# Kernel optimization log

Hardware: AMD Instinct MI355X
Metric: run time of the kernel (lower is better)

Reference implementation:

```python
import jax, jax.numpy as jnp
import numpy as np

N_NODES = 100000
N_EDGES = 1200000
D_FEAT = 64


def setup_inputs() -> dict:
    key = jax.random.key(0)
    k1, k2, k3 = jax.random.split(key, 3)
    x = jax.random.normal(k1, (N_NODES, D_FEAT), dtype=jnp.float32)
    edge_index = jax.random.randint(k2, (2, N_EDGES), 0, N_NODES, dtype=jnp.int64)
    edge_weight = jax.random.uniform(k3, (N_EDGES, 1), dtype=jnp.float32)
    return {"x": x, "edge_index": edge_index, "edge_weight": edge_weight}


def reference(x, edge_index, edge_weight):
    # flow = source_to_target: j = edge_index[0] (source), i = edge_index[1] (target)
    src, dst = edge_index[0], edge_index[1]
    # message: x_j  (gather along node_dim=-2)
    msg = x[src]                       # [E, D]
    # aggregate: scatter-'sum' with edge_weight scaling
    msg = msg * edge_weight            # [E, D]
    out = jax.ops.segment_sum(msg, dst, num_segments=N_NODES)  # [N, D]
    # update: identity
    return out
```

## Files before the change

### kernel.cpp

```cpp
#include <hip/hip_runtime.h>
#include <hip/hip_bf16.h>


constexpr int D_FEAT        = 64;
constexpr int BIN_SHIFT     = 7;
constexpr int NODES_PER_BIN = 1 << BIN_SHIFT;
constexpr int NBINS_MAX     = 1024;
constexpr int BIN_CAP       = 2048;
constexpr int EPB           = 4096;
constexpr int OVF_CAP       = 32768;

__device__ __forceinline__ int wave_incl_scan(int v, int lane) {
    #pragma unroll
    for (int d = 1; d < 64; d <<= 1) {
        int t = __shfl_up(v, d);
        if (lane >= d) v += t;
    }
    return v;
}

__device__ __forceinline__ unsigned short f32_to_bf16_rn(float f) {
    unsigned int u = __float_as_uint(f);
    u += 0x7FFFu + ((u >> 16) & 1u);
    return (unsigned short)(u >> 16);
}

__global__ __launch_bounds__(256) void mp_convert(
    const float* __restrict__ x, ushort* __restrict__ xb, int n4)
{
    const int i = blockIdx.x * blockDim.x + threadIdx.x;
    if (i < n4) {
        const float4 v = reinterpret_cast<const float4*>(x)[i];
        ushort4 o;
        o.x = f32_to_bf16_rn(v.x);
        o.y = f32_to_bf16_rn(v.y);
        o.z = f32_to_bf16_rn(v.z);
        o.w = f32_to_bf16_rn(v.w);
        reinterpret_cast<ushort4*>(xb)[i] = o;
    }
}

__global__ __launch_bounds__(1024) void mp_partition(
    const int* __restrict__ src, const int* __restrict__ dst,
    const float* __restrict__ w,
    int*  __restrict__ gcnt,
    int2* __restrict__ payload,
    int*  __restrict__ ovf_cnt, int4* __restrict__ ovf,
    int n_edges, int nbins)
{
    __shared__ int cnt[NBINS_MAX];
    __shared__ int start[NBINS_MAX];
    __shared__ int cur[NBINS_MAX];
    __shared__ int gbase[NBINS_MAX];
    __shared__ unsigned short binof[EPB];
    __shared__ int2 sorted[EPB];
    __shared__ int wsum[16];

    const int t    = threadIdx.x;
    const int lane = t & 63;
    const int wid  = t >> 6;
    const int base = blockIdx.x * EPB;
    const int nblk = min(EPB, n_edges - base);

    if (t < NBINS_MAX) cnt[t] = 0;
    __syncthreads();

    const int i4 = (base >> 2) + t;
    int4 d4 = make_int4(0, 0, 0, 0);
    bool have = (i4 * 4 < n_edges);
    if (have) {
        d4 = reinterpret_cast<const int4*>(dst)[i4];
        atomicAdd(&cnt[d4.x >> BIN_SHIFT], 1);
        atomicAdd(&cnt[d4.y >> BIN_SHIFT], 1);
        atomicAdd(&cnt[d4.z >> BIN_SHIFT], 1);
        atomicAdd(&cnt[d4.w >> BIN_SHIFT], 1);
    }
    __syncthreads();

    const int c = (t < nbins) ? cnt[t] : 0;
    const int incl = wave_incl_scan(c, lane);
    if (lane == 63) wsum[wid] = incl;
    __syncthreads();
    int woff = 0;
    #pragma unroll
    for (int k = 0; k < 16; ++k) woff += (k < wid) ? wsum[k] : 0;
    const int excl = woff + incl - c;
    if (t < nbins) {
        start[t] = excl;
        cur[t]   = excl;
        if (c > 0) gbase[t] = atomicAdd(&gcnt[t], c);
    }
    __syncthreads();

    if (have) {
        const int4   s4 = reinterpret_cast<const int4*>(src)[i4];
        const float4 w4 = reinterpret_cast<const float4*>(w)[i4];
        const int   dd[4] = {d4.x, d4.y, d4.z, d4.w};
        const int   ss[4] = {s4.x, s4.y, s4.z, s4.w};
        const float ww[4] = {w4.x, w4.y, w4.z, w4.w};
        #pragma unroll
        for (int j = 0; j < 4; ++j) {
            const int b   = dd[j] >> BIN_SHIFT;
            const int low = dd[j] & (NODES_PER_BIN - 1);
            const int p   = atomicAdd(&cur[b], 1);
            sorted[p] = make_int2((low << 20) | ss[j], __float_as_int(ww[j]));
            binof[p]  = (unsigned short)b;
        }
    }
    __syncthreads();

    #pragma unroll
    for (int k = 0; k < EPB / 1024; ++k) {
        const int i = k * 1024 + t;
        if (i >= nblk) break;
        const int b    = binof[i];
        const int idx  = i - start[b];
        const int gpos = gbase[b] + idx;
        const int2 e   = sorted[i];
        if (gpos < BIN_CAP) {
            payload[(size_t)b * BIN_CAP + gpos] = e;
        } else {
            const int op = atomicAdd(ovf_cnt, 1);
            if (op < OVF_CAP)
                ovf[op] = make_int4((b << BIN_SHIFT) + (e.x >> 20),
                                    e.x & 0xFFFFF, e.y, 0);
        }
    }
}

__global__ __launch_bounds__(512) void mp_bin_gather(
    const ushort* __restrict__ xb,
    const float*  __restrict__ x,
    const int*  __restrict__ gcnt,
    const int2* __restrict__ payload,
    const int*  __restrict__ ovf_cnt, const int4* __restrict__ ovf,
    float* __restrict__ out, int n_nodes)
{
    __shared__ int2 sraw[BIN_CAP];
    __shared__ int2 sedge[BIN_CAP];
    __shared__ int ncnt[NODES_PER_BIN];
    __shared__ int nstart[NODES_PER_BIN + 1];
    __shared__ int ncur[NODES_PER_BIN];

    const int b    = blockIdx.x;
    const int t    = threadIdx.x;
    const int lane = t & 63;
    const int wid  = t >> 6;
    const int sub  = lane >> 3;
    const int fg   = (lane & 7) * 8;

    const int m = min(gcnt[b], BIN_CAP);
    const int2* pl = payload + (size_t)b * BIN_CAP;

    for (int i = t; i < NODES_PER_BIN; i += 512) ncnt[i] = 0;
    __syncthreads();

    for (int i = t; i < m; i += 512) {
        const int2 e = pl[i];
        sraw[i] = e;
        atomicAdd(&ncnt[e.x >> 20], 1);
    }
    __syncthreads();

    if (t < 64) {
        const int a0 = ncnt[t], a1 = ncnt[64 + t];
        const int s0 = wave_incl_scan(a0, t);
        const int s1 = wave_incl_scan(a1, t);
        const int tot0 = __shfl(s0, 63);
        nstart[t]      = s0 - a0;
        nstart[64 + t] = tot0 + s1 - a1;
        if (t == 63) nstart[128] = tot0 + s1;
    }
    __syncthreads();
    for (int i = t; i < NODES_PER_BIN; i += 512) ncur[i] = nstart[i];
    __syncthreads();

    for (int i = t; i < m; i += 512) {
        const int2 e = sraw[i];
        const int p  = atomicAdd(&ncur[e.x >> 20], 1);
        sedge[p] = e;
    }
    __syncthreads();

    const int novf = *ovf_cnt;

    for (int n = wid; n < NODES_PER_BIN; n += 8) {
        const int node = (b << BIN_SHIFT) + n;
        if (node >= n_nodes) break;
        const int s0 = nstart[n], s1 = nstart[n + 1];

        float a0 = 0.f, a1 = 0.f, a2 = 0.f, a3 = 0.f;
        float a4 = 0.f, a5 = 0.f, a6 = 0.f, a7 = 0.f;

        int base = s0;
        for (; base + 8 <= s1; base += 8) {
            const int2 p = sedge[base + sub];
            const uint4 xv = *reinterpret_cast<const uint4*>(
                xb + (size_t)(p.x & 0xFFFFF) * D_FEAT + fg);
            const float ww = __int_as_float(p.y);
            a0 = fmaf(__uint_as_float(xv.x << 16),          ww, a0);
            a1 = fmaf(__uint_as_float(xv.x & 0xFFFF0000u),  ww, a1);
            a2 = fmaf(__uint_as_float(xv.y << 16),          ww, a2);
            a3 = fmaf(__uint_as_float(xv.y & 0xFFFF0000u),  ww, a3);
            a4 = fmaf(__uint_as_float(xv.z << 16),          ww, a4);
            a5 = fmaf(__uint_as_float(xv.z & 0xFFFF0000u),  ww, a5);
            a6 = fmaf(__uint_as_float(xv.w << 16),          ww, a6);
            a7 = fmaf(__uint_as_float(xv.w & 0xFFFF0000u),  ww, a7);
        }
        const int rem = s1 - base;
        if (sub < rem) {
            const int2 p = sedge[base + sub];
            const uint4 xv = *reinterpret_cast<const uint4*>(
                xb + (size_t)(p.x & 0xFFFFF) * D_FEAT + fg);
            const float ww = __int_as_float(p.y);
            a0 = fmaf(__uint_as_float(xv.x << 16),          ww, a0);
            a1 = fmaf(__uint_as_float(xv.x & 0xFFFF0000u),  ww, a1);
            a2 = fmaf(__uint_as_float(xv.y << 16),          ww, a2);
            a3 = fmaf(__uint_as_float(xv.y & 0xFFFF0000u),  ww, a3);
            a4 = fmaf(__uint_as_float(xv.z << 16),          ww, a4);
            a5 = fmaf(__uint_as_float(xv.z & 0xFFFF0000u),  ww, a5);
            a6 = fmaf(__uint_as_float(xv.w << 16),          ww, a6);
            a7 = fmaf(__uint_as_float(xv.w & 0xFFFF0000u),  ww, a7);
        }

        #pragma unroll
        for (int mask = 8; mask <= 32; mask <<= 1) {
            a0 += __shfl_xor(a0, mask); a1 += __shfl_xor(a1, mask);
            a2 += __shfl_xor(a2, mask); a3 += __shfl_xor(a3, mask);
            a4 += __shfl_xor(a4, mask); a5 += __shfl_xor(a5, mask);
            a6 += __shfl_xor(a6, mask); a7 += __shfl_xor(a7, mask);
        }

        if (sub == 0) {
            if (novf > 0) {
                const int lim = min(novf, OVF_CAP);
                for (int j = 0; j < lim; ++j) {
                    const int4 o = ovf[j];
                    if (o.x == node) {
                        const float* xr = x + (size_t)o.y * D_FEAT + fg;
                        const float ww = __int_as_float(o.z);
                        a0 = fmaf(xr[0], ww, a0); a1 = fmaf(xr[1], ww, a1);
                        a2 = fmaf(xr[2], ww, a2); a3 = fmaf(xr[3], ww, a3);
                        a4 = fmaf(xr[4], ww, a4); a5 = fmaf(xr[5], ww, a5);
                        a6 = fmaf(xr[6], ww, a6); a7 = fmaf(xr[7], ww, a7);
                    }
                }
            }
            float* orow = out + (size_t)node * D_FEAT + fg;
            *reinterpret_cast<float4*>(orow)     = make_float4(a0, a1, a2, a3);
            *reinterpret_cast<float4*>(orow + 4) = make_float4(a4, a5, a6, a7);
        }
    }
}

__global__ __launch_bounds__(256) void mp_scatter_atomic(
    const float* __restrict__ x, const int* __restrict__ src,
    const int* __restrict__ dst, const float* __restrict__ w,
    float* __restrict__ out, int n_edges)
{
    const int gtid = blockIdx.x * blockDim.x + threadIdx.x;
    const int edge = gtid >> 6;
    const int lane = threadIdx.x & 63;
    if (edge >= n_edges) return;
    const int s = src[edge];
    const int d = dst[edge];
    const float ww = w[edge];
    atomicAdd(&out[(size_t)d * D_FEAT + lane], x[(size_t)s * D_FEAT + lane] * ww);
}

extern "C" void kernel_launch(void* const* d_in, const int* in_sizes, int n_in,
                              void* d_out, int out_size, void* d_ws, size_t ws_size,
                              hipStream_t stream)
{
    const float* x          = (const float*)d_in[0];
    const int*   edge_index = (const int*)d_in[1];
    const float* w          = (const float*)d_in[2];
    float*       out        = (float*)d_out;

    const int n_edges = in_sizes[1] / 2;
    const int n_nodes = in_sizes[0] / D_FEAT;
    const int* src = edge_index;
    const int* dst = edge_index + n_edges;

    const int nbins = (n_nodes + NODES_PER_BIN - 1) >> BIN_SHIFT;

    int*    gcnt    = (int*)d_ws;
    int*    ovf_cnt = gcnt + NBINS_MAX;
    int4*   ovf     = (int4*)(gcnt + NBINS_MAX + 64);
    int2*   payload = (int2*)(ovf + OVF_CAP);
    ushort* xb      = (ushort*)(payload + (size_t)nbins * BIN_CAP);
    const size_t need = (size_t)(NBINS_MAX + 64) * 4 + (size_t)OVF_CAP * 16
                      + (size_t)nbins * BIN_CAP * 8
                      + (size_t)n_nodes * D_FEAT * 2;

    const bool ok = (ws_size >= need) && (nbins <= NBINS_MAX) && ((n_edges & 3) == 0);

    if (ok) {
        hipMemsetAsync(gcnt, 0, (size_t)(NBINS_MAX + 64) * 4, stream);
        const int n4 = n_nodes * D_FEAT / 4;
        mp_convert<<<(n4 + 255) / 256, 256, 0, stream>>>(x, xb, n4);
        const int g1 = (n_edges + EPB - 1) / EPB;
        mp_partition<<<g1, 1024, 0, stream>>>(src, dst, w, gcnt, payload,
                                              ovf_cnt, ovf, n_edges, nbins);
        mp_bin_gather<<<nbins, 512, 0, stream>>>(xb, x, gcnt, payload,
                                                 ovf_cnt, ovf, out, n_nodes);
        return;
    }

    hipMemsetAsync(d_out, 0, (size_t)out_size * sizeof(float), stream);
    const int grid = (int)(((size_t)n_edges * 64 + 255) / 256);
    mp_scatter_atomic<<<grid, 256, 0, stream>>>(x, src, dst, w, out, n_edges);
}
```

Measured before the change: 146.0 us.

## Fuse bf16 conversion into partition kernel and assign one node per 8-lane group

The fp32-to-bf16 conversion of x moves into the partition kernel as a grid-stride loop, which removes one kernel launch. The gather stage is also remapped so that each 8-lane subgroup owns a whole node instead of a full wave sharing one node, with two edges processed per iteration. This drops the cross-lane shuffle reduction and the per-node idle lanes. In exchange, work is less balanced across lanes when degrees vary, each lane does serial per-node loops that are less coalesced, and the overflow scan now runs on every lane.

```diff
diff --git a/kernel.cpp b/kernel.cpp
--- a/kernel.cpp
+++ b/kernel.cpp
@@ -25,24 +25,10 @@
     return (unsigned short)(u >> 16);
 }
 
-__global__ __launch_bounds__(256) void mp_convert(
-    const float* __restrict__ x, ushort* __restrict__ xb, int n4)
-{
-    const int i = blockIdx.x * blockDim.x + threadIdx.x;
-    if (i < n4) {
-        const float4 v = reinterpret_cast<const float4*>(x)[i];
-        ushort4 o;
-        o.x = f32_to_bf16_rn(v.x);
-        o.y = f32_to_bf16_rn(v.y);
-        o.z = f32_to_bf16_rn(v.z);
-        o.w = f32_to_bf16_rn(v.w);
-        reinterpret_cast<ushort4*>(xb)[i] = o;
-    }
-}
-
 __global__ __launch_bounds__(1024) void mp_partition(
     const int* __restrict__ src, const int* __restrict__ dst,
-    const float* __restrict__ w,
+    const float* __restrict__ w, const float* __restrict__ x,
+    ushort* __restrict__ xb, int n4,
     int*  __restrict__ gcnt,
     int2* __restrict__ payload,
     int*  __restrict__ ovf_cnt, int4* __restrict__ ovf,
@@ -61,6 +47,16 @@
     const int wid  = t >> 6;
     const int base = blockIdx.x * EPB;
     const int nblk = min(EPB, n_edges - base);
+
+    for (int i = blockIdx.x * 1024 + t; i < n4; i += gridDim.x * 1024) {
+        const float4 v = reinterpret_cast<const float4*>(x)[i];
+        ushort4 o;
+        o.x = f32_to_bf16_rn(v.x);
+        o.y = f32_to_bf16_rn(v.y);
+        o.z = f32_to_bf16_rn(v.z);
+        o.w = f32_to_bf16_rn(v.w);
+        reinterpret_cast<ushort4*>(xb)[i] = o;
+    }
 
     if (t < NBINS_MAX) cnt[t] = 0;
     __syncthreads();
@@ -147,7 +143,8 @@
     const int lane = t & 63;
     const int wid  = t >> 6;
     const int sub  = lane >> 3;
-    const int fg   = (lane & 7) * 8;
+    const int fq   = lane & 7;
+    const int fg   = fq * 8;
 
     const int m = min(gcnt[b], BIN_CAP);
     const int2* pl = payload + (size_t)b * BIN_CAP;
@@ -184,54 +181,59 @@
 
     const int novf = *ovf_cnt;
 
-    for (int n = wid; n < NODES_PER_BIN; n += 8) {
+    #pragma unroll
+    for (int nb = 0; nb < 16; nb += 8) {
+        const int n    = wid * 16 + nb + sub;
         const int node = (b << BIN_SHIFT) + n;
-        if (node >= n_nodes) break;
-        const int s0 = nstart[n], s1 = nstart[n + 1];
+        const int s0 = nstart[n];
+        const int s1 = nstart[n + 1];
 
         float a0 = 0.f, a1 = 0.f, a2 = 0.f, a3 = 0.f;
         float a4 = 0.f, a5 = 0.f, a6 = 0.f, a7 = 0.f;
 
-        int base = s0;
-        for (; base + 8 <= s1; base += 8) {
-            const int2 p = sedge[base + sub];
+        int e = s0;
+        for (; e + 2 <= s1; e += 2) {
+            const int2 pA = sedge[e];
+            const int2 pB = sedge[e + 1];
+            const uint4 xA = *reinterpret_cast<const uint4*>(
+                xb + (size_t)(pA.x & 0xFFFFF) * D_FEAT + fg);
+            const uint4 xB = *reinterpret_cast<const uint4*>(
+                xb + (size_t)(pB.x & 0xFFFFF) * D_FEAT + fg);
+            const float wA = __int_as_float(pA.y);
+            const float wB = __int_as_float(pB.y);
+            a0 = fmaf(__uint_as_float(xA.x << 16),         wA, a0);
+            a1 = fmaf(__uint_as_float(xA.x & 0xFFFF0000u), wA, a1);
+            a2 = fmaf(__uint_as_float(xA.y << 16),         wA, a2);
+            a3 = fmaf(__uint_as_float(xA.y & 0xFFFF0000u), wA, a3);
+            a4 = fmaf(__uint_as_float(xA.z << 16),         wA, a4);
+            a5 = fmaf(__uint_as_float(xA.z & 0xFFFF0000u), wA, a5);
+            a6 = fmaf(__uint_as_float(xA.w << 16),         wA, a6);
+            a7 = fmaf(__uint_as_float(xA.w & 0xFFFF0000u), wA, a7);
+            a0 = fmaf(__uint_as_float(xB.x << 16),         wB, a0);
+            a1 = fmaf(__uint_as_float(xB.x & 0xFFFF0000u), wB, a1);
+            a2 = fmaf(__uint_as_float(xB.y << 16),         wB, a2);
+            a3 = fmaf(__uint_as_float(xB.y & 0xFFFF0000u), wB, a3);
+            a4 = fmaf(__uint_as_float(xB.z << 16),         wB, a4);
+            a5 = fmaf(__uint_as_float(xB.z & 0xFFFF0000u), wB, a5);
+            a6 = fmaf(__uint_as_float(xB.w << 16),         wB, a6);
+            a7 = fmaf(__uint_as_float(xB.w & 0xFFFF0000u), wB, a7);
+        }
+        if (e < s1) {
+            const int2 p = sedge[e];
             const uint4 xv = *reinterpret_cast<const uint4*>(
                 xb + (size_t)(p.x & 0xFFFFF) * D_FEAT + fg);
             const float ww = __int_as_float(p.y);
-            a0 = fmaf(__uint_as_float(xv.x << 16),          ww, a0);
-            a1 = fmaf(__uint_as_float(xv.x & 0xFFFF0000u),  ww, a1);
-            a2 = fmaf(__uint_as_float(xv.y << 16),          ww, a2);
-            a3 = fmaf(__uint_as_float(xv.y & 0xFFFF0000u),  ww, a3);
-            a4 = fmaf(__uint_as_float(xv.z << 16),          ww, a4);
-            a5 = fmaf(__uint_as_float(xv.z & 0xFFFF0000u),  ww, a5);
-            a6 = fmaf(__uint_as_float(xv.w << 16),          ww, a6);
-            a7 = fmaf(__uint_as_float(xv.w & 0xFFFF0000u),  ww, a7);
-        }
-        const int rem = s1 - base;
-        if (sub < rem) {
-            const int2 p = sedge[base + sub];
-            const uint4 xv = *reinterpret_cast<const uint4*>(
-                xb + (size_t)(p.x & 0xFFFFF) * D_FEAT + fg);
-            const float ww = __int_as_float(p.y);
-            a0 = fmaf(__uint_as_float(xv.x << 16),          ww, a0);
-            a1 = fmaf(__uint_as_float(xv.x & 0xFFFF0000u),  ww, a1);
-            a2 = fmaf(__uint_as_float(xv.y << 16),          ww, a2);
-            a3 = fmaf(__uint_as_float(xv.y & 0xFFFF0000u),  ww, a3);
-            a4 = fmaf(__uint_as_float(xv.z << 16),          ww, a4);
-            a5 = fmaf(__uint_as_float(xv.z & 0xFFFF0000u),  ww, a5);
-            a6 = fmaf(__uint_as_float(xv.w << 16),          ww, a6);
-            a7 = fmaf(__uint_as_float(xv.w & 0xFFFF0000u),  ww, a7);
-        }
-
-        #pragma unroll
-        for (int mask = 8; mask <= 32; mask <<= 1) {
-            a0 += __shfl_xor(a0, mask); a1 += __shfl_xor(a1, mask);
-            a2 += __shfl_xor(a2, mask); a3 += __shfl_xor(a3, mask);
-            a4 += __shfl_xor(a4, mask); a5 += __shfl_xor(a5, mask);
-            a6 += __shfl_xor(a6, mask); a7 += __shfl_xor(a7, mask);
-        }
-
-        if (sub == 0) {
+            a0 = fmaf(__uint_as_float(xv.x << 16),         ww, a0);
+            a1 = fmaf(__uint_as_float(xv.x & 0xFFFF0000u), ww, a1);
+            a2 = fmaf(__uint_as_float(xv.y << 16),         ww, a2);
+            a3 = fmaf(__uint_as_float(xv.y & 0xFFFF0000u), ww, a3);
+            a4 = fmaf(__uint_as_float(xv.z << 16),         ww, a4);
+            a5 = fmaf(__uint_as_float(xv.z & 0xFFFF0000u), ww, a5);
+            a6 = fmaf(__uint_as_float(xv.w << 16),         ww, a6);
+            a7 = fmaf(__uint_as_float(xv.w & 0xFFFF0000u), ww, a7);
+        }
+
+        if (node < n_nodes) {
             if (novf > 0) {
                 const int lim = min(novf, OVF_CAP);
                 for (int j = 0; j < lim; ++j) {
@@ -293,15 +295,16 @@
                       + (size_t)nbins * BIN_CAP * 8
                       + (size_t)n_nodes * D_FEAT * 2;
 
-    const bool ok = (ws_size >= need) && (nbins <= NBINS_MAX) && ((n_edges & 3) == 0);
+    const bool ok = (ws_size >= need) && (nbins <= NBINS_MAX) && ((n_edges & 3) == 0)
+                 && ((n_nodes * D_FEAT) % 4 == 0);
 
     if (ok) {
         hipMemsetAsync(gcnt, 0, (size_t)(NBINS_MAX + 64) * 4, stream);
         const int n4 = n_nodes * D_FEAT / 4;
-        mp_convert<<<(n4 + 255) / 256, 256, 0, stream>>>(x, xb, n4);
         const int g1 = (n_edges + EPB - 1) / EPB;
-        mp_partition<<<g1, 1024, 0, stream>>>(src, dst, w, gcnt, payload,
-                                              ovf_cnt, ovf, n_edges, nbins);
+        mp_partition<<<g1, 1024, 0, stream>>>(src, dst, w, x, xb, n4,
+                                              gcnt, payload, ovf_cnt, ovf,
+                                              n_edges, nbins);
         mp_bin_gather<<<nbins, 512, 0, stream>>>(xb, x, gcnt, payload,
                                                  ovf_cnt, ovf, out, n_nodes);
         return;
```

Result: faster. 123.8 us (-15.2%).
